# Kernel optimization log

Hardware: AMD Instinct MI355X
Metric: run time of the kernel (lower is better)

## Reference

```python
import jax, jax.numpy as jnp
import numpy as np

HID = 2560
NH, P, N, G, K = 80, 64, 128, 1, 4
INTER = NH * P            # 5120
CONV_DIM = INTER + 2 * G * N  # 5376
PROJ = INTER + CONV_DIM + NH  # 10576
EPS = 1e-5
DT_MIN, DT_MAX = 0.0, 100.0
BATCH = 64


def setup_inputs() -> dict:
    key = jax.random.key(0)
    ks = jax.random.split(key, 11)
    return {
        "input_states": jax.random.normal(ks[0], (BATCH, 1, HID), jnp.float32),
        "conv_state": 0.1 * jax.random.normal(ks[1], (BATCH, CONV_DIM, K), jnp.float32),
        "ssm_state": 0.1 * jax.random.normal(ks[2], (BATCH, NH, P, N), jnp.float32),
        "in_proj_w": jax.random.normal(ks[3], (PROJ, HID), jnp.float32) * (HID ** -0.5),
        "conv_w": jax.random.normal(ks[4], (CONV_DIM, K), jnp.float32) * 0.2,
        "conv_b": jax.random.normal(ks[5], (CONV_DIM,), jnp.float32) * 0.02,
        "dt_bias": jax.random.normal(ks[6], (NH,), jnp.float32) * 0.1,
        "A_log": jnp.log(jnp.arange(1, NH + 1, dtype=jnp.float32)),
        "D": jnp.ones((NH,), jnp.float32),
        "norm_w": jnp.ones((INTER,), jnp.float32),
        "out_proj_w": jax.random.normal(ks[7], (HID, INTER), jnp.float32) * (INTER ** -0.5),
    }


def reference(input_states, conv_state, ssm_state, in_proj_w, conv_w, conv_b,
              dt_bias, A_log, D, norm_w, out_proj_w):
    B = input_states.shape[0]
    # in_proj: (B,1,HID) @ (HID,PROJ) -> (B,1,PROJ); d_mlp == 0 with these dims
    proj = jnp.einsum("bsh,ph->bsp", input_states, in_proj_w)
    gate = proj[..., :INTER]                       # (B,1,INTER)
    hBC = proj[..., INTER:INTER + CONV_DIM]        # (B,1,CONV_DIM)
    dt = proj[..., INTER + CONV_DIM:]              # (B,1,NH)

    # conv cache update: roll left, append current token
    new_conv_state = jnp.concatenate(
        [conv_state[:, :, 1:], hBC[:, 0, :, None]], axis=-1)  # (B,CONV_DIM,K)
    x = jnp.sum(new_conv_state * conv_w[None], axis=-1) + conv_b  # (B,CONV_DIM)
    x = jax.nn.silu(x)

    hs = x[:, :INTER].reshape(B, NH, P)            # (B,NH,P)
    Bm = x[:, INTER:INTER + G * N].reshape(B, G, N)
    Cm = x[:, INTER + G * N:].reshape(B, G, N)
    Bm = jnp.repeat(Bm, NH // G, axis=1)           # (B,NH,N)
    Cm = jnp.repeat(Cm, NH // G, axis=1)           # (B,NH,N)

    # discretization (dt is per-head, broadcast over head_dim as in source)
    dt_sp = jnp.clip(jax.nn.softplus(dt[:, 0, :] + dt_bias), DT_MIN, DT_MAX)  # (B,NH)
    A = -jnp.exp(A_log)                            # (NH,)
    dA = jnp.exp(dt_sp * A)                        # (B,NH)

    dBx = dt_sp[:, :, None, None] * Bm[:, :, None, :] * hs[..., None]  # (B,NH,P,N)
    new_ssm = ssm_state * dA[:, :, None, None] + dBx                   # (B,NH,P,N)

    y = jnp.einsum("bhpn,bhn->bhp", new_ssm, Cm)   # (B,NH,P)
    y = y + hs * D[None, :, None]
    y = y.reshape(B, 1, INTER)

    # gated RMSNorm (fp32 internals)
    yf = y.astype(jnp.float32) * jax.nn.silu(gate.astype(jnp.float32))
    var = jnp.mean(yf * yf, axis=-1, keepdims=True)
    yn = norm_w * (yf * jax.lax.rsqrt(var + EPS)).astype(y.dtype)

    out = jnp.einsum("bsi,hi->bsh", yn, out_proj_w)  # (B,1,HID)
    return out
```

## Files before the change

### kernel.cpp

```cpp
#include <hip/hip_runtime.h>
#include <stdint.h>

#define HID 2560
#define NH 80
#define PDIM 64
#define NDIM 128
#define INTER 5120
#define CONV_DIM 5376
#define PROJ_DIM 10576
#define NBATCH 64
#define EPS_ 1e-5f

typedef short short8 __attribute__((ext_vector_type(8)));
typedef float f32x4 __attribute__((ext_vector_type(4)));

__device__ __forceinline__ unsigned short f2bf(float f){
  unsigned u = __builtin_bit_cast(unsigned, f);
  u += 0x7FFFu + ((u >> 16) & 1u);
  return (unsigned short)(u >> 16);
}
__device__ __forceinline__ float silu_(float x){ return x / (1.f + __expf(-x)); }

__global__ __launch_bounds__(256) void k_dt(const float* __restrict__ X,
                                            const float* __restrict__ W,
                                            float* __restrict__ dt_part,
                                            unsigned short* __restrict__ Xb){
  const int h = blockIdx.x, ks = blockIdx.y;
  const int tid = threadIdx.x, wid = tid >> 6, lane = tid & 63;
  const float* wr = W + (size_t)(INTER + CONV_DIM + h) * HID + ks * 320;
  float w[5];
  #pragma unroll
  for (int i = 0; i < 5; ++i) w[i] = wr[lane + i * 64];
  #pragma unroll
  for (int bi = 0; bi < 16; ++bi){
    const int b = wid * 16 + bi;
    const float* xr = X + (size_t)b * HID + ks * 320;
    float x[5];
    float acc = 0.f;
    #pragma unroll
    for (int i = 0; i < 5; ++i){ x[i] = xr[lane + i * 64]; acc += x[i] * w[i]; }
    if (h == 0){
      #pragma unroll
      for (int i = 0; i < 5; ++i)
        Xb[(size_t)b * HID + ks * 320 + lane + i * 64] = f2bf(x[i]);
    }
    #pragma unroll
    for (int m = 32; m; m >>= 1) acc += __shfl_xor(acc, m);
    if (lane == 0) dt_part[(ks * NBATCH + b) * NH + h] = acc;
  }
}

__global__ __launch_bounds__(64, 1) void k1_proj(const unsigned short* __restrict__ Xb,
                                                 const float* __restrict__ W,
                                                 float* __restrict__ pp){
  const int lane = threadIdx.x;
  const int lr = lane & 15, lg = lane >> 4;
  const int n0 = blockIdx.x * 64;
  const int ks = blockIdx.y;
  const int kb = ks * 320;
  const short* ap = (const short*)Xb + (size_t)lr * HID + kb + lg * 8;
  const float* bp0; const float* bp1; const float* bp2; const float* bp3;
  {
    int r0 = n0;          if (r0 > PROJ_DIM - 16) r0 = PROJ_DIM - 16;
    int r1 = n0 + 16;     if (r1 > PROJ_DIM - 16) r1 = PROJ_DIM - 16;
    int r2 = n0 + 32;     if (r2 > PROJ_DIM - 16) r2 = PROJ_DIM - 16;
    int r3 = n0 + 48;     if (r3 > PROJ_DIM - 16) r3 = PROJ_DIM - 16;
    bp0 = W + (size_t)(r0 + lr) * HID + kb + lg * 8;
    bp1 = W + (size_t)(r1 + lr) * HID + kb + lg * 8;
    bp2 = W + (size_t)(r2 + lr) * HID + kb + lg * 8;
    bp3 = W + (size_t)(r3 + lr) * HID + kb + lg * 8;
  }
  f32x4 acc0[4], acc1[4], acc2[4], acc3[4];
  #pragma unroll
  for (int mt = 0; mt < 4; ++mt){
    acc0[mt] = (f32x4){0,0,0,0}; acc1[mt] = (f32x4){0,0,0,0};
    acc2[mt] = (f32x4){0,0,0,0}; acc3[mt] = (f32x4){0,0,0,0};
  }
  short8 A0[2], A1[2], A2[2], A3[2];
  float4 Bv0[2][2], Bv1[2][2], Bv2[2][2], Bv3[2][2];
  A0[0] = *(const short8*)(ap);
  A1[0] = *(const short8*)(ap + 16 * HID);
  A2[0] = *(const short8*)(ap + 32 * HID);
  A3[0] = *(const short8*)(ap + 48 * HID);
  Bv0[0][0] = *(const float4*)(bp0); Bv0[0][1] = *(const float4*)(bp0 + 4);
  Bv1[0][0] = *(const float4*)(bp1); Bv1[0][1] = *(const float4*)(bp1 + 4);
  Bv2[0][0] = *(const float4*)(bp2); Bv2[0][1] = *(const float4*)(bp2 + 4);
  Bv3[0][0] = *(const float4*)(bp3); Bv3[0][1] = *(const float4*)(bp3 + 4);
  #pragma unroll
  for (int s = 0; s < 10; ++s){
    const int p = s & 1;
    if (s + 1 < 10){
      const int k = (s + 1) * 32, q = p ^ 1;
      A0[q] = *(const short8*)(ap + k);
      A1[q] = *(const short8*)(ap + 16 * HID + k);
      A2[q] = *(const short8*)(ap + 32 * HID + k);
      A3[q] = *(const short8*)(ap + 48 * HID + k);
      Bv0[q][0] = *(const float4*)(bp0 + k); Bv0[q][1] = *(const float4*)(bp0 + k + 4);
      Bv1[q][0] = *(const float4*)(bp1 + k); Bv1[q][1] = *(const float4*)(bp1 + k + 4);
      Bv2[q][0] = *(const float4*)(bp2 + k); Bv2[q][1] = *(const float4*)(bp2 + k + 4);
      Bv3[q][0] = *(const float4*)(bp3 + k); Bv3[q][1] = *(const float4*)(bp3 + k + 4);
    }
    short8 bb0, bb1, bb2, bb3;
    bb0[0]=(short)f2bf(Bv0[p][0].x); bb0[1]=(short)f2bf(Bv0[p][0].y);
    bb0[2]=(short)f2bf(Bv0[p][0].z); bb0[3]=(short)f2bf(Bv0[p][0].w);
    bb0[4]=(short)f2bf(Bv0[p][1].x); bb0[5]=(short)f2bf(Bv0[p][1].y);
    bb0[6]=(short)f2bf(Bv0[p][1].z); bb0[7]=(short)f2bf(Bv0[p][1].w);
    bb1[0]=(short)f2bf(Bv1[p][0].x); bb1[1]=(short)f2bf(Bv1[p][0].y);
    bb1[2]=(short)f2bf(Bv1[p][0].z); bb1[3]=(short)f2bf(Bv1[p][0].w);
    bb1[4]=(short)f2bf(Bv1[p][1].x); bb1[5]=(short)f2bf(Bv1[p][1].y);
    bb1[6]=(short)f2bf(Bv1[p][1].z); bb1[7]=(short)f2bf(Bv1[p][1].w);
    bb2[0]=(short)f2bf(Bv2[p][0].x); bb2[1]=(short)f2bf(Bv2[p][0].y);
    bb2[2]=(short)f2bf(Bv2[p][0].z); bb2[3]=(short)f2bf(Bv2[p][0].w);
    bb2[4]=(short)f2bf(Bv2[p][1].x); bb2[5]=(short)f2bf(Bv2[p][1].y);
    bb2[6]=(short)f2bf(Bv2[p][1].z); bb2[7]=(short)f2bf(Bv2[p][1].w);
    bb3[0]=(short)f2bf(Bv3[p][0].x); bb3[1]=(short)f2bf(Bv3[p][0].y);
    bb3[2]=(short)f2bf(Bv3[p][0].z); bb3[3]=(short)f2bf(Bv3[p][0].w);
    bb3[4]=(short)f2bf(Bv3[p][1].x); bb3[5]=(short)f2bf(Bv3[p][1].y);
    bb3[6]=(short)f2bf(Bv3[p][1].z); bb3[7]=(short)f2bf(Bv3[p][1].w);
    acc0[0] = __builtin_amdgcn_mfma_f32_16x16x32_bf16(A0[p], bb0, acc0[0], 0, 0, 0);
    acc0[1] = __builtin_amdgcn_mfma_f32_16x16x32_bf16(A1[p], bb0, acc0[1], 0, 0, 0);
    acc0[2] = __builtin_amdgcn_mfma_f32_16x16x32_bf16(A2[p], bb0, acc0[2], 0, 0, 0);
    acc0[3] = __builtin_amdgcn_mfma_f32_16x16x32_bf16(A3[p], bb0, acc0[3], 0, 0, 0);
    acc1[0] = __builtin_amdgcn_mfma_f32_16x16x32_bf16(A0[p], bb1, acc1[0], 0, 0, 0);
    acc1[1] = __builtin_amdgcn_mfma_f32_16x16x32_bf16(A1[p], bb1, acc1[1], 0, 0, 0);
    acc1[2] = __builtin_amdgcn_mfma_f32_16x16x32_bf16(A2[p], bb1, acc1[2], 0, 0, 0);
    acc1[3] = __builtin_amdgcn_mfma_f32_16x16x32_bf16(A3[p], bb1, acc1[3], 0, 0, 0);
    acc2[0] = __builtin_amdgcn_mfma_f32_16x16x32_bf16(A0[p], bb2, acc2[0], 0, 0, 0);
    acc2[1] = __builtin_amdgcn_mfma_f32_16x16x32_bf16(A1[p], bb2, acc2[1], 0, 0, 0);
    acc2[2] = __builtin_amdgcn_mfma_f32_16x16x32_bf16(A2[p], bb2, acc2[2], 0, 0, 0);
    acc2[3] = __builtin_amdgcn_mfma_f32_16x16x32_bf16(A3[p], bb2, acc2[3], 0, 0, 0);
    acc3[0] = __builtin_amdgcn_mfma_f32_16x16x32_bf16(A0[p], bb3, acc3[0], 0, 0, 0);
    acc3[1] = __builtin_amdgcn_mfma_f32_16x16x32_bf16(A1[p], bb3, acc3[1], 0, 0, 0);
    acc3[2] = __builtin_amdgcn_mfma_f32_16x16x32_bf16(A2[p], bb3, acc3[2], 0, 0, 0);
    acc3[3] = __builtin_amdgcn_mfma_f32_16x16x32_bf16(A3[p], bb3, acc3[3], 0, 0, 0);
  }
  float* plane = pp + (size_t)ks * NBATCH * PROJ_DIM;
  #pragma unroll
  for (int mt = 0; mt < 4; ++mt){
    #pragma unroll
    for (int r = 0; r < 4; ++r){
      const int m = mt * 16 + lg * 4 + r;
      float* pm = plane + (size_t)m * PROJ_DIM;
      if (n0      < PROJ_DIM) pm[n0      + lr] = acc0[mt][r];
      if (n0 + 16 < PROJ_DIM) pm[n0 + 16 + lr] = acc1[mt][r];
      if (n0 + 32 < PROJ_DIM) pm[n0 + 32 + lr] = acc2[mt][r];
      if (n0 + 48 < PROJ_DIM) pm[n0 + 48 + lr] = acc3[mt][r];
    }
  }
}

__global__ __launch_bounds__(256) void k2a(const float* __restrict__ cs,
                                           const float* __restrict__ cw,
                                           const float* __restrict__ cb,
                                           const float* __restrict__ pp,
                                           const float* __restrict__ dt_part,
                                           const float* __restrict__ dt_bias,
                                           const float* __restrict__ A_log,
                                           float* __restrict__ hs_bc,
                                           float* __restrict__ dt_sp,
                                           float* __restrict__ dAv,
                                           float* __restrict__ s_bc){
  const int b = blockIdx.y;
  const int c0 = blockIdx.x * 384;
  const int tid = threadIdx.x;
  const size_t plane = (size_t)NBATCH * PROJ_DIM;
  __shared__ float bc[384];
  for (int i = tid; i < 384; i += 256){
    const int c = c0 + i;
    float4 s4 = *(const float4*)(cs + ((size_t)b * CONV_DIM + c) * 4);
    float4 w4 = *(const float4*)(cw + (size_t)c * 4);
    const size_t pidx = (size_t)b * PROJ_DIM + INTER + c;
    float hbc = 0.f;
    #pragma unroll
    for (int ks = 0; ks < 8; ++ks) hbc += pp[(size_t)ks * plane + pidx];
    float x = s4.y * w4.x + s4.z * w4.y + s4.w * w4.z + hbc * w4.w + cb[c];
    float v = silu_(x);
    hs_bc[(size_t)b * CONV_DIM + c] = v;
    if (blockIdx.x == 13) bc[i] = v;
  }
  if (blockIdx.x == 0 && tid < NH){
    float acc = dt_bias[tid];
    #pragma unroll
    for (int ks = 0; ks < 8; ++ks) acc += dt_part[(ks * NBATCH + b) * NH + tid];
    float sp = acc > 15.f ? acc : log1pf(__expf(acc));
    sp = fminf(fmaxf(sp, 0.f), 100.f);
    dt_sp[b * NH + tid] = sp;
    dAv[b * NH + tid] = __expf(-sp * __expf(A_log[tid]));
  }
  if (blockIdx.x == 13){
    __syncthreads();
    if (tid < 64){
      float p = bc[128 + tid] * bc[256 + tid] + bc[192 + tid] * bc[320 + tid];
      #pragma unroll
      for (int m = 32; m; m >>= 1) p += __shfl_xor(p, m);
      if (tid == 0) s_bc[b] = p;
    }
  }
}

__global__ __launch_bounds__(256) void k2b(const float* __restrict__ ssm,
                                           const float* __restrict__ hs_bc,
                                           const float* __restrict__ pp,
                                           const float* __restrict__ dt_sp,
                                           const float* __restrict__ dAv,
                                           const float* __restrict__ s_bc,
                                           const float* __restrict__ Dp,
                                           const float* __restrict__ norm_w,
                                           unsigned short* __restrict__ yfb,
                                           float* __restrict__ ssq_part){
  const int h = blockIdx.x, b = blockIdx.y;
  const int tid = threadIdx.x;
  const int wid = tid >> 6, lane = tid & 63;
  const int lr = lane & 15, lg = lane >> 4;
  const float dA_s = dAv[b * NH + h];
  const float coef = dt_sp[b * NH + h] * s_bc[b] + Dp[h];
  const size_t plane = (size_t)NBATCH * PROJ_DIM;
  const float* Cb = hs_bc + (size_t)b * CONV_DIM + INTER + NDIM;
  float4 c0 = *(const float4*)(Cb + lr * 8);
  float4 c1 = *(const float4*)(Cb + lr * 8 + 4);
  const float* srow = ssm + ((size_t)b * NH + h) * PDIM * NDIM;
  float ssq = 0.f;
  __shared__ float ssql[4];
  #pragma unroll
  for (int r = 0; r < 4; ++r){
    const int p = wid * 16 + r * 4 + lg;
    const float* sp_ = srow + (size_t)p * NDIM + lr * 8;
    float4 v0 = *(const float4*)(sp_);
    float4 v1 = *(const float4*)(sp_ + 4);
    float dot = v0.x*c0.x + v0.y*c0.y + v0.z*c0.z + v0.w*c0.w
              + v1.x*c1.x + v1.y*c1.y + v1.z*c1.z + v1.w*c1.w;
    dot += __shfl_xor(dot, 1); dot += __shfl_xor(dot, 2);
    dot += __shfl_xor(dot, 4); dot += __shfl_xor(dot, 8);
    if (lr == 0){
      const int hp = h * PDIM + p;
      float hs = hs_bc[(size_t)b * CONV_DIM + hp];
      float y = dA_s * dot + hs * coef;
      const size_t gi = (size_t)b * PROJ_DIM + hp;
      float g = 0.f;
      #pragma unroll
      for (int ks = 0; ks < 8; ++ks) g += pp[(size_t)ks * plane + gi];
      float yf = y * silu_(g) * norm_w[hp];
      yfb[(size_t)b * INTER + hp] = f2bf(yf);
      ssq += yf * yf;
    }
  }
  #pragma unroll
  for (int m = 32; m; m >>= 1) ssq += __shfl_xor(ssq, m);
  if (lane == 0) ssql[wid] = ssq;
  __syncthreads();
  if (tid == 0) ssq_part[b * NH + h] = ssql[0] + ssql[1] + ssql[2] + ssql[3];
}

__global__ __launch_bounds__(64, 1) void k3_out(const unsigned short* __restrict__ Yb,
                                                const float* __restrict__ W,
                                                float* __restrict__ part){
  const int lane = threadIdx.x;
  const int lr = lane & 15, lg = lane >> 4;
  const int n0 = blockIdx.x * 16;
  const int ks = blockIdx.y;
  const int kb = ks * 1280;
  const short* ap = (const short*)Yb + (size_t)lr * INTER + kb + lg * 8;
  const float* bp = W + (size_t)(n0 + lr) * INTER + kb + lg * 8;
  f32x4 acc0 = {0,0,0,0}, acc1 = {0,0,0,0}, acc2 = {0,0,0,0}, acc3 = {0,0,0,0};
  short8 A0[4], A1[4], A2[4], A3[4];
  float4 B0[4], B1[4];
  #pragma unroll
  for (int p = 0; p < 4; ++p){
    const int k = p * 32;
    A0[p] = *(const short8*)(ap + k);
    A1[p] = *(const short8*)(ap + 16 * INTER + k);
    A2[p] = *(const short8*)(ap + 32 * INTER + k);
    A3[p] = *(const short8*)(ap + 48 * INTER + k);
    B0[p] = *(const float4*)(bp + k);
    B1[p] = *(const float4*)(bp + k + 4);
  }
  #pragma unroll 4
  for (int s = 0; s < 36; ++s){
    const int p = s & 3;
    short8 bb;
    bb[0]=(short)f2bf(B0[p].x); bb[1]=(short)f2bf(B0[p].y);
    bb[2]=(short)f2bf(B0[p].z); bb[3]=(short)f2bf(B0[p].w);
    bb[4]=(short)f2bf(B1[p].x); bb[5]=(short)f2bf(B1[p].y);
    bb[6]=(short)f2bf(B1[p].z); bb[7]=(short)f2bf(B1[p].w);
    acc0 = __builtin_amdgcn_mfma_f32_16x16x32_bf16(A0[p], bb, acc0, 0, 0, 0);
    acc1 = __builtin_amdgcn_mfma_f32_16x16x32_bf16(A1[p], bb, acc1, 0, 0, 0);
    acc2 = __builtin_amdgcn_mfma_f32_16x16x32_bf16(A2[p], bb, acc2, 0, 0, 0);
    acc3 = __builtin_amdgcn_mfma_f32_16x16x32_bf16(A3[p], bb, acc3, 0, 0, 0);
    const int k = (s + 4) * 32;
    A0[p] = *(const short8*)(ap + k);
    A1[p] = *(const short8*)(ap + 16 * INTER + k);
    A2[p] = *(const short8*)(ap + 32 * INTER + k);
    A3[p] = *(const short8*)(ap + 48 * INTER + k);
    B0[p] = *(const float4*)(bp + k);
    B1[p] = *(const float4*)(bp + k + 4);
  }
  #pragma unroll
  for (int s = 36; s < 40; ++s){
    const int p = s & 3;
    short8 bb;
    bb[0]=(short)f2bf(B0[p].x); bb[1]=(short)f2bf(B0[p].y);
    bb[2]=(short)f2bf(B0[p].z); bb[3]=(short)f2bf(B0[p].w);
    bb[4]=(short)f2bf(B1[p].x); bb[5]=(short)f2bf(B1[p].y);
    bb[6]=(short)f2bf(B1[p].z); bb[7]=(short)f2bf(B1[p].w);
    acc0 = __builtin_amdgcn_mfma_f32_16x16x32_bf16(A0[p], bb, acc0, 0, 0, 0);
    acc1 = __builtin_amdgcn_mfma_f32_16x16x32_bf16(A1[p], bb, acc1, 0, 0, 0);
    acc2 = __builtin_amdgcn_mfma_f32_16x16x32_bf16(A2[p], bb, acc2, 0, 0, 0);
    acc3 = __builtin_amdgcn_mfma_f32_16x16x32_bf16(A3[p], bb, acc3, 0, 0, 0);
  }
  float* pt = part + (size_t)ks * NBATCH * 2560;
  #pragma unroll
  for (int r = 0; r < 4; ++r){
    const int m = lg * 4 + r;
    pt[(size_t)(m     ) * 2560 + n0 + lr] = acc0[r];
    pt[(size_t)(m + 16) * 2560 + n0 + lr] = acc1[r];
    pt[(size_t)(m + 32) * 2560 + n0 + lr] = acc2[r];
    pt[(size_t)(m + 48) * 2560 + n0 + lr] = acc3[r];
  }
}

__global__ __launch_bounds__(256) void k4_norm(const float* __restrict__ part,
                                               const float* __restrict__ ssq_part,
                                               float* __restrict__ out){
  const int b = blockIdx.y;
  const int tid = threadIdx.x;
  __shared__ float w4[4];
  __shared__ float sc;
  float v = (tid < NH) ? ssq_part[b * NH + tid] : 0.f;
  #pragma unroll
  for (int m = 32; m; m >>= 1) v += __shfl_xor(v, m);
  const int wid = tid >> 6, lane = tid & 63;
  if (lane == 0) w4[wid] = v;
  __syncthreads();
  if (tid == 0){
    float total = w4[0] + w4[1] + w4[2] + w4[3];
    sc = rsqrtf(total / (float)INTER + EPS_);
  }
  __syncthreads();
  const int j = blockIdx.x * 256 + tid;
  const size_t idx = (size_t)b * 2560 + j;
  const size_t plane = (size_t)NBATCH * 2560;
  float s = part[idx] + part[plane + idx] + part[2*plane + idx] + part[3*plane + idx];
  out[idx] = sc * s;
}

extern "C" void kernel_launch(void* const* d_in, const int* in_sizes, int n_in,
                              void* d_out, int out_size, void* d_ws, size_t ws_size,
                              hipStream_t stream){
  const float* x_in       = (const float*)d_in[0];
  const float* conv_state = (const float*)d_in[1];
  const float* ssm_state  = (const float*)d_in[2];
  const float* in_proj_w  = (const float*)d_in[3];
  const float* conv_w     = (const float*)d_in[4];
  const float* conv_b     = (const float*)d_in[5];
  const float* dt_bias    = (const float*)d_in[6];
  const float* A_log      = (const float*)d_in[7];
  const float* Dp         = (const float*)d_in[8];
  const float* norm_w     = (const float*)d_in[9];
  const float* out_proj_w = (const float*)d_in[10];
  float* out = (float*)d_out;

  char* ws = (char*)d_ws;
  unsigned short* Xb   = (unsigned short*)(ws);
  float* dt_part       = (float*)(ws + 327680);
  float* pp            = (float*)(ws + 491520);
  float* hs_bc         = (float*)(ws + 22151168);
  float* dt_sp         = (float*)(ws + 23527424);
  float* dAv           = (float*)(ws + 23547904);
  float* s_bc          = (float*)(ws + 23568384);
  float* ssq           = (float*)(ws + 23568640);
  unsigned short* Yb   = (unsigned short*)(ws + 23589120);
  float* part          = (float*)(ws + 24244480);

  k_dt<<<dim3(NH, 8), dim3(256), 0, stream>>>(x_in, in_proj_w, dt_part, Xb);
  k1_proj<<<dim3(166, 8), dim3(64), 0, stream>>>(Xb, in_proj_w, pp);
  k2a<<<dim3(14, NBATCH), dim3(256), 0, stream>>>(conv_state, conv_w, conv_b, pp,
                                                  dt_part, dt_bias, A_log,
                                                  hs_bc, dt_sp, dAv, s_bc);
  k2b<<<dim3(NH, NBATCH), dim3(256), 0, stream>>>(ssm_state, hs_bc, pp, dt_sp, dAv,
                                                  s_bc, Dp, norm_w, Yb, ssq);
  k3_out<<<dim3(160, 4), dim3(64), 0, stream>>>(Yb, out_proj_w, part);
  k4_norm<<<dim3(10, NBATCH), dim3(256), 0, stream>>>(part, ssq, out);
}
```

Measured before the change: 127.5 us.

## Retile out-projection GEMM to 32-column tiles with 16-way split-K

Each k3_out block now covers 32 output columns instead of 16, and the K dimension is split 16 ways (320 per block) instead of 4. The grid grows from 640 to 1280 single-wave blocks, and the in-flight loads switch to a 2-stage double buffer. This spreads the memory-bound fp32 weight stream across more blocks and lets each loaded A fragment feed twice as many MFMAs. In exchange, the partial-sum buffer grows fourfold, k4_norm must read 16 planes, and the workspace must be large enough to hold them.

```diff
diff --git a/kernel.cpp b/kernel.cpp
--- a/kernel.cpp
+++ b/kernel.cpp
@@ -256,65 +256,65 @@
                                                 float* __restrict__ part){
   const int lane = threadIdx.x;
   const int lr = lane & 15, lg = lane >> 4;
-  const int n0 = blockIdx.x * 16;
+  const int n0 = blockIdx.x * 32;
   const int ks = blockIdx.y;
-  const int kb = ks * 1280;
+  const int kb = ks * 320;
   const short* ap = (const short*)Yb + (size_t)lr * INTER + kb + lg * 8;
-  const float* bp = W + (size_t)(n0 + lr) * INTER + kb + lg * 8;
-  f32x4 acc0 = {0,0,0,0}, acc1 = {0,0,0,0}, acc2 = {0,0,0,0}, acc3 = {0,0,0,0};
-  short8 A0[4], A1[4], A2[4], A3[4];
-  float4 B0[4], B1[4];
-  #pragma unroll
-  for (int p = 0; p < 4; ++p){
-    const int k = p * 32;
-    A0[p] = *(const short8*)(ap + k);
-    A1[p] = *(const short8*)(ap + 16 * INTER + k);
-    A2[p] = *(const short8*)(ap + 32 * INTER + k);
-    A3[p] = *(const short8*)(ap + 48 * INTER + k);
-    B0[p] = *(const float4*)(bp + k);
-    B1[p] = *(const float4*)(bp + k + 4);
-  }
-  #pragma unroll 4
-  for (int s = 0; s < 36; ++s){
-    const int p = s & 3;
-    short8 bb;
-    bb[0]=(short)f2bf(B0[p].x); bb[1]=(short)f2bf(B0[p].y);
-    bb[2]=(short)f2bf(B0[p].z); bb[3]=(short)f2bf(B0[p].w);
-    bb[4]=(short)f2bf(B1[p].x); bb[5]=(short)f2bf(B1[p].y);
-    bb[6]=(short)f2bf(B1[p].z); bb[7]=(short)f2bf(B1[p].w);
-    acc0 = __builtin_amdgcn_mfma_f32_16x16x32_bf16(A0[p], bb, acc0, 0, 0, 0);
-    acc1 = __builtin_amdgcn_mfma_f32_16x16x32_bf16(A1[p], bb, acc1, 0, 0, 0);
-    acc2 = __builtin_amdgcn_mfma_f32_16x16x32_bf16(A2[p], bb, acc2, 0, 0, 0);
-    acc3 = __builtin_amdgcn_mfma_f32_16x16x32_bf16(A3[p], bb, acc3, 0, 0, 0);
-    const int k = (s + 4) * 32;
-    A0[p] = *(const short8*)(ap + k);
-    A1[p] = *(const short8*)(ap + 16 * INTER + k);
-    A2[p] = *(const short8*)(ap + 32 * INTER + k);
-    A3[p] = *(const short8*)(ap + 48 * INTER + k);
-    B0[p] = *(const float4*)(bp + k);
-    B1[p] = *(const float4*)(bp + k + 4);
-  }
-  #pragma unroll
-  for (int s = 36; s < 40; ++s){
-    const int p = s & 3;
-    short8 bb;
-    bb[0]=(short)f2bf(B0[p].x); bb[1]=(short)f2bf(B0[p].y);
-    bb[2]=(short)f2bf(B0[p].z); bb[3]=(short)f2bf(B0[p].w);
-    bb[4]=(short)f2bf(B1[p].x); bb[5]=(short)f2bf(B1[p].y);
-    bb[6]=(short)f2bf(B1[p].z); bb[7]=(short)f2bf(B1[p].w);
-    acc0 = __builtin_amdgcn_mfma_f32_16x16x32_bf16(A0[p], bb, acc0, 0, 0, 0);
-    acc1 = __builtin_amdgcn_mfma_f32_16x16x32_bf16(A1[p], bb, acc1, 0, 0, 0);
-    acc2 = __builtin_amdgcn_mfma_f32_16x16x32_bf16(A2[p], bb, acc2, 0, 0, 0);
-    acc3 = __builtin_amdgcn_mfma_f32_16x16x32_bf16(A3[p], bb, acc3, 0, 0, 0);
+  const float* bp0 = W + (size_t)(n0      + lr) * INTER + kb + lg * 8;
+  const float* bp1 = W + (size_t)(n0 + 16 + lr) * INTER + kb + lg * 8;
+  f32x4 acc0[4], acc1[4];
+  #pragma unroll
+  for (int mt = 0; mt < 4; ++mt){
+    acc0[mt] = (f32x4){0,0,0,0}; acc1[mt] = (f32x4){0,0,0,0};
+  }
+  short8 A0[2], A1[2], A2[2], A3[2];
+  float4 Bv0[2][2], Bv1[2][2];
+  A0[0] = *(const short8*)(ap);
+  A1[0] = *(const short8*)(ap + 16 * INTER);
+  A2[0] = *(const short8*)(ap + 32 * INTER);
+  A3[0] = *(const short8*)(ap + 48 * INTER);
+  Bv0[0][0] = *(const float4*)(bp0); Bv0[0][1] = *(const float4*)(bp0 + 4);
+  Bv1[0][0] = *(const float4*)(bp1); Bv1[0][1] = *(const float4*)(bp1 + 4);
+  #pragma unroll
+  for (int s = 0; s < 10; ++s){
+    const int p = s & 1;
+    if (s + 1 < 10){
+      const int k = (s + 1) * 32, q = p ^ 1;
+      A0[q] = *(const short8*)(ap + k);
+      A1[q] = *(const short8*)(ap + 16 * INTER + k);
+      A2[q] = *(const short8*)(ap + 32 * INTER + k);
+      A3[q] = *(const short8*)(ap + 48 * INTER + k);
+      Bv0[q][0] = *(const float4*)(bp0 + k); Bv0[q][1] = *(const float4*)(bp0 + k + 4);
+      Bv1[q][0] = *(const float4*)(bp1 + k); Bv1[q][1] = *(const float4*)(bp1 + k + 4);
+    }
+    short8 bb0, bb1;
+    bb0[0]=(short)f2bf(Bv0[p][0].x); bb0[1]=(short)f2bf(Bv0[p][0].y);
+    bb0[2]=(short)f2bf(Bv0[p][0].z); bb0[3]=(short)f2bf(Bv0[p][0].w);
+    bb0[4]=(short)f2bf(Bv0[p][1].x); bb0[5]=(short)f2bf(Bv0[p][1].y);
+    bb0[6]=(short)f2bf(Bv0[p][1].z); bb0[7]=(short)f2bf(Bv0[p][1].w);
+    bb1[0]=(short)f2bf(Bv1[p][0].x); bb1[1]=(short)f2bf(Bv1[p][0].y);
+    bb1[2]=(short)f2bf(Bv1[p][0].z); bb1[3]=(short)f2bf(Bv1[p][0].w);
+    bb1[4]=(short)f2bf(Bv1[p][1].x); bb1[5]=(short)f2bf(Bv1[p][1].y);
+    bb1[6]=(short)f2bf(Bv1[p][1].z); bb1[7]=(short)f2bf(Bv1[p][1].w);
+    acc0[0] = __builtin_amdgcn_mfma_f32_16x16x32_bf16(A0[p], bb0, acc0[0], 0, 0, 0);
+    acc0[1] = __builtin_amdgcn_mfma_f32_16x16x32_bf16(A1[p], bb0, acc0[1], 0, 0, 0);
+    acc0[2] = __builtin_amdgcn_mfma_f32_16x16x32_bf16(A2[p], bb0, acc0[2], 0, 0, 0);
+    acc0[3] = __builtin_amdgcn_mfma_f32_16x16x32_bf16(A3[p], bb0, acc0[3], 0, 0, 0);
+    acc1[0] = __builtin_amdgcn_mfma_f32_16x16x32_bf16(A0[p], bb1, acc1[0], 0, 0, 0);
+    acc1[1] = __builtin_amdgcn_mfma_f32_16x16x32_bf16(A1[p], bb1, acc1[1], 0, 0, 0);
+    acc1[2] = __builtin_amdgcn_mfma_f32_16x16x32_bf16(A2[p], bb1, acc1[2], 0, 0, 0);
+    acc1[3] = __builtin_amdgcn_mfma_f32_16x16x32_bf16(A3[p], bb1, acc1[3], 0, 0, 0);
   }
   float* pt = part + (size_t)ks * NBATCH * 2560;
   #pragma unroll
-  for (int r = 0; r < 4; ++r){
-    const int m = lg * 4 + r;
-    pt[(size_t)(m     ) * 2560 + n0 + lr] = acc0[r];
-    pt[(size_t)(m + 16) * 2560 + n0 + lr] = acc1[r];
-    pt[(size_t)(m + 32) * 2560 + n0 + lr] = acc2[r];
-    pt[(size_t)(m + 48) * 2560 + n0 + lr] = acc3[r];
+  for (int mt = 0; mt < 4; ++mt){
+    #pragma unroll
+    for (int r = 0; r < 4; ++r){
+      const int m = mt * 16 + lg * 4 + r;
+      float* pm = pt + (size_t)m * 2560;
+      pm[n0      + lr] = acc0[mt][r];
+      pm[n0 + 16 + lr] = acc1[mt][r];
+    }
   }
 }
 
@@ -339,7 +339,9 @@
   const int j = blockIdx.x * 256 + tid;
   const size_t idx = (size_t)b * 2560 + j;
   const size_t plane = (size_t)NBATCH * 2560;
-  float s = part[idx] + part[plane + idx] + part[2*plane + idx] + part[3*plane + idx];
+  float s = 0.f;
+  #pragma unroll
+  for (int ks = 0; ks < 16; ++ks) s += part[(size_t)ks * plane + idx];
   out[idx] = sc * s;
 }
 
@@ -378,6 +380,6 @@
                                                   hs_bc, dt_sp, dAv, s_bc);
   k2b<<<dim3(NH, NBATCH), dim3(256), 0, stream>>>(ssm_state, hs_bc, pp, dt_sp, dAv,
                                                   s_bc, Dp, norm_w, Yb, ssq);
-  k3_out<<<dim3(160, 4), dim3(64), 0, stream>>>(Yb, out_proj_w, part);
+  k3_out<<<dim3(80, 16), dim3(64), 0, stream>>>(Yb, out_proj_w, part);
   k4_norm<<<dim3(10, NBATCH), dim3(256), 0, stream>>>(part, ssq, out);
 }
```

New measurement: 123.7 us, median of 2. 3.0% less time.
